# Kernel optimization log

Hardware: AMD Instinct MI355X
Metric: run time of the kernel (lower is better)

The kernel has to match this reference:

```python
import jax, jax.numpy as jnp
import numpy as np

OUT_FEATURES = 4096
IN_FEATURES = 4096
K = 4096
BLOCK_SIZE = 8
NUM_BLOCKS = OUT_FEATURES * IN_FEATURES // BLOCK_SIZE  # 2,097,152
ORIGINAL_NUMEL = OUT_FEATURES * IN_FEATURES


def setup_inputs() -> dict:
    key = jax.random.key(0)
    k1, k2, k3, k4 = jax.random.split(key, 4)
    x = jax.random.normal(k1, (4, 2048, IN_FEATURES), dtype=jnp.float32)
    codebook = jax.random.normal(k2, (K, BLOCK_SIZE), dtype=jnp.float32)
    indices = jax.random.randint(k3, (NUM_BLOCKS,), 0, K, dtype=jnp.int64)
    bias = jax.random.normal(k4, (OUT_FEATURES,), dtype=jnp.float32)
    return {"x": x, "codebook": codebook, "indices": indices, "bias": bias}


def reference(x, codebook, indices, bias):
    # Reconstruct weight from codebook: gather blocks, flatten, slice, reshape.
    reconstructed = codebook[indices]                      # [num_blocks, block_size]
    W = reconstructed.reshape(-1)[:ORIGINAL_NUMEL]
    W = W.reshape(OUT_FEATURES, IN_FEATURES)               # [out, in]
    # F.linear: x @ W^T + bias
    return jnp.einsum('bsi,oi->bso', x, W) + bias
```

## Files before the change

### kernel.cpp

```cpp
#include <hip/hip_runtime.h>
#include <stdint.h>


#define M_DIM 8192
#define N_DIM 4096
#define K_DIM 4096
#define BM 256
#define BN 256
#define BK 64
#define NT (K_DIM / BK)
#define NUM_W_BLOCKS 2097152
#define W_WGS (NUM_W_BLOCKS / 256)
#define X_WGS ((M_DIM * K_DIM / 4) / 256)

typedef __attribute__((ext_vector_type(8))) __bf16 bf16x8;
typedef __attribute__((ext_vector_type(4))) float floatx4;
typedef __attribute__((ext_vector_type(2))) unsigned int uintx2;

__device__ __forceinline__ unsigned int f2bf(float f) {
    unsigned int u = __builtin_bit_cast(unsigned int, f);
    u += 0x7fffu + ((u >> 16) & 1u);
    return u >> 16;
}

__global__ __launch_bounds__(256) void prep_kernel(
    const float* __restrict__ cb, const int* __restrict__ idx,
    uint4* __restrict__ W, const floatx4* __restrict__ x,
    uintx2* __restrict__ xb) {
    const int wg = blockIdx.x;
    if (wg < W_WGS) {
        const int b = wg * 256 + threadIdx.x;
        const int id = __builtin_nontemporal_load(idx + b);
        const float4* s = (const float4*)(cb + ((size_t)id << 3));
        const float4 a = s[0];
        const float4 c = s[1];
        uint4 o;
        o.x = f2bf(a.x) | (f2bf(a.y) << 16);
        o.y = f2bf(a.z) | (f2bf(a.w) << 16);
        o.z = f2bf(c.x) | (f2bf(c.y) << 16);
        o.w = f2bf(c.z) | (f2bf(c.w) << 16);
        W[b] = o;
    } else {
        const size_t t = (size_t)(wg - W_WGS) * 256 + threadIdx.x;
        const floatx4 a = __builtin_nontemporal_load(x + t);
        uintx2 o;
        o.x = f2bf(a.x) | (f2bf(a.y) << 16);
        o.y = f2bf(a.z) | (f2bf(a.w) << 16);
        xb[t] = o;
    }
}

__device__ __forceinline__ void async_copy16(const __bf16* g, __bf16* s) {
    __builtin_amdgcn_global_load_lds(
        (const __attribute__((address_space(1))) unsigned int*)(uintptr_t)g,
        (__attribute__((address_space(3))) unsigned int*)(uintptr_t)s,
        16, 0, 0);
}

#define STAGE(gsrc, arr, slotElems)                                        \
    do {                                                                   \
        async_copy16((gsrc), (arr) + (slotElems) + wave512);               \
        async_copy16((gsrc) + (size_t)128 * K_DIM,                         \
                     (arr) + (slotElems) + 4096 + wave512);                \
    } while (0)

__global__ __launch_bounds__(512, 2) void gemm_bt_kernel(
    const __bf16* __restrict__ A,
    const __bf16* __restrict__ B,
    const float* __restrict__ bias,
    float* __restrict__ C) {
    __shared__ __align__(16) __bf16 sA[4 * 8192];
    __shared__ __align__(16) __bf16 sB[4 * 8192];

    const int tid = threadIdx.x;
    const int wave = tid >> 6;
    const int lane = tid & 63;
    const int wr = wave >> 2;
    const int wc = wave & 3;

    const int flat = blockIdx.x;
    const int swz = (flat & 7) * 64 + (flat >> 3);
    const int m0 = (swz & 31) * BM;
    const int n0 = (swz >> 5) * BN;

    const int srow = tid >> 2;
    const int schunk = ((tid & 3) ^ ((srow >> 1) & 3)) << 3;
    const __bf16* gA = A + (size_t)(m0 + srow) * K_DIM + schunk;
    const __bf16* gB = B + (size_t)(n0 + srow) * K_DIM + schunk;
    const int wave512 = wave << 9;

    const int fr = lane & 15;
    const int roff = fr * 32 + (((lane >> 4) ^ ((fr >> 1) & 3)) << 3);
    const int aBase = wr * 4096 + roff;
    const int bBase = wc * 2048 + roff;

    floatx4 acc[8][4] = {};

    STAGE(gA, sA, 0);
    STAGE(gB, sB, 0);
    STAGE(gA + 32, sA, 8192);
    STAGE(gB + 32, sB, 8192);
    STAGE(gA + 64, sA, 16384);
    STAGE(gB + 64, sB, 16384);
    asm volatile("s_waitcnt vmcnt(4)" ::: "memory");
    __builtin_amdgcn_s_barrier();

    for (int t = 0; t < NT; ++t) {
        const int cs = (t & 1) ? 16384 : 0;
        const int ns = cs ^ 16384;
        const __bf16* sA0 = sA + cs;
        const __bf16* sA1 = sA + cs + 8192;
        const __bf16* sB0 = sB + cs;
        const __bf16* sB1 = sB + cs + 8192;

        bf16x8 af[4], bfr[4];

#pragma unroll
        for (int i = 0; i < 4; ++i)
            af[i] = *(const bf16x8*)(sA0 + aBase + i * 512);
#pragma unroll
        for (int j = 0; j < 4; ++j)
            bfr[j] = *(const bf16x8*)(sB0 + bBase + j * 512);
        if (t + 1 < NT) { STAGE(gA + (size_t)(t + 1) * 64 + 32, sA, ns + 8192); }
        __builtin_amdgcn_s_barrier();
        asm volatile("s_waitcnt lgkmcnt(0)" ::: "memory");
        __builtin_amdgcn_s_setprio(1);
#pragma unroll
        for (int i = 0; i < 4; ++i)
#pragma unroll
            for (int j = 0; j < 4; ++j)
                acc[i][j] = __builtin_amdgcn_mfma_f32_16x16x32_bf16(
                    af[i], bfr[j], acc[i][j], 0, 0, 0);
        __builtin_amdgcn_s_setprio(0);
        __builtin_amdgcn_s_barrier();

#pragma unroll
        for (int i = 0; i < 4; ++i)
            af[i] = *(const bf16x8*)(sA0 + aBase + 2048 + i * 512);
        if (t + 1 < NT) { STAGE(gB + (size_t)(t + 1) * 64 + 32, sB, ns + 8192); }
        __builtin_amdgcn_s_barrier();
        asm volatile("s_waitcnt lgkmcnt(0)" ::: "memory");
        __builtin_amdgcn_s_setprio(1);
#pragma unroll
        for (int i = 0; i < 4; ++i)
#pragma unroll
            for (int j = 0; j < 4; ++j)
                acc[i + 4][j] = __builtin_amdgcn_mfma_f32_16x16x32_bf16(
                    af[i], bfr[j], acc[i + 4][j], 0, 0, 0);
        __builtin_amdgcn_s_setprio(0);
        __builtin_amdgcn_s_barrier();

#pragma unroll
        for (int i = 0; i < 4; ++i)
            af[i] = *(const bf16x8*)(sA1 + aBase + i * 512);
#pragma unroll
        for (int j = 0; j < 4; ++j)
            bfr[j] = *(const bf16x8*)(sB1 + bBase + j * 512);
        if (t + 2 < NT) { STAGE(gA + (size_t)(t + 2) * 64, sA, cs); }
        __builtin_amdgcn_s_barrier();
        asm volatile("s_waitcnt lgkmcnt(0)" ::: "memory");
        __builtin_amdgcn_s_setprio(1);
#pragma unroll
        for (int i = 0; i < 4; ++i)
#pragma unroll
            for (int j = 0; j < 4; ++j)
                acc[i][j] = __builtin_amdgcn_mfma_f32_16x16x32_bf16(
                    af[i], bfr[j], acc[i][j], 0, 0, 0);
        __builtin_amdgcn_s_setprio(0);
        __builtin_amdgcn_s_barrier();

#pragma unroll
        for (int i = 0; i < 4; ++i)
            af[i] = *(const bf16x8*)(sA1 + aBase + 2048 + i * 512);
        if (t + 2 < NT) { STAGE(gB + (size_t)(t + 2) * 64, sB, cs); }
        __builtin_amdgcn_s_barrier();
        asm volatile("s_waitcnt lgkmcnt(0)" ::: "memory");
        __builtin_amdgcn_s_setprio(1);
#pragma unroll
        for (int i = 0; i < 4; ++i)
#pragma unroll
            for (int j = 0; j < 4; ++j)
                acc[i + 4][j] = __builtin_amdgcn_mfma_f32_16x16x32_bf16(
                    af[i], bfr[j], acc[i + 4][j], 0, 0, 0);
        __builtin_amdgcn_s_setprio(0);
        if (t < NT - 2)
            asm volatile("s_waitcnt vmcnt(4)" ::: "memory");
        else
            asm volatile("s_waitcnt vmcnt(0)" ::: "memory");
        __builtin_amdgcn_s_barrier();
    }

    const int crow = (lane >> 4) * 4;
    const int ccol = lane & 15;
#pragma unroll
    for (int j = 0; j < 4; ++j) {
        const int n = n0 + wc * 64 + j * 16 + ccol;
        const float bv = bias[n];
#pragma unroll
        for (int i = 0; i < 8; ++i) {
            const int m = m0 + wr * 128 + i * 16 + crow;
            float* cp = C + (size_t)m * N_DIM + n;
#pragma unroll
            for (int r = 0; r < 4; ++r)
                __builtin_nontemporal_store(acc[i][j][r] + bv,
                                            cp + (size_t)r * N_DIM);
        }
    }
}

extern "C" void kernel_launch(void* const* d_in, const int* in_sizes, int n_in,
                              void* d_out, int out_size, void* d_ws, size_t ws_size,
                              hipStream_t stream) {
    const float* x    = (const float*)d_in[0];
    const float* cb   = (const float*)d_in[1];
    const int*   idx  = (const int*)d_in[2];
    const float* bias = (const float*)d_in[3];
    float* out = (float*)d_out;

    __bf16* Wb = (__bf16*)d_ws;
    __bf16* Xb = (__bf16*)((char*)d_ws + (size_t)N_DIM * K_DIM * sizeof(__bf16));

    prep_kernel<<<W_WGS + X_WGS, 256, 0, stream>>>(
        cb, idx, (uint4*)Wb, (const floatx4*)x, (uintx2*)Xb);

    dim3 grid(M_DIM / BM * (N_DIM / BN));
    gemm_bt_kernel<<<grid, 512, 0, stream>>>(Xb, Wb, bias, out);
}
```

Baseline: 468.9 us.

## Use persistent-style prep loops, remap GEMM tile order, relax vmcnt waits

The prep kernel moves from one element per thread to a fixed grid of workgroups that loop over several elements, and the x conversion now writes 16-byte bf16 chunks instead of 8-byte ones. The GEMM block-to-tile mapping is changed so each XCD works on a compact 4x8 patch of M/N tiles, to improve L2 reuse. The vmcnt waits are relaxed so more async global-to-LDS copies stay in flight between half-iterations. The risk is that the looser waits could break the pipeline ordering or reduce overlap if they are counted wrong.

```diff
diff --git a/kernel.cpp b/kernel.cpp
--- a/kernel.cpp
+++ b/kernel.cpp
@@ -10,12 +10,15 @@
 #define BK 64
 #define NT (K_DIM / BK)
 #define NUM_W_BLOCKS 2097152
-#define W_WGS (NUM_W_BLOCKS / 256)
-#define X_WGS ((M_DIM * K_DIM / 4) / 256)
+
+#define PW_WGS 512
+#define PW_ITERS (NUM_W_BLOCKS / (PW_WGS * 256 * 4))
+#define PX_WGS 2048
+#define PX_OUT (M_DIM * K_DIM / 8)
+#define PX_ITERS (PX_OUT / (PX_WGS * 256))
 
 typedef __attribute__((ext_vector_type(8))) __bf16 bf16x8;
 typedef __attribute__((ext_vector_type(4))) float floatx4;
-typedef __attribute__((ext_vector_type(2))) unsigned int uintx2;
 
 __device__ __forceinline__ unsigned int f2bf(float f) {
     unsigned int u = __builtin_bit_cast(unsigned int, f);
@@ -25,28 +28,42 @@
 
 __global__ __launch_bounds__(256) void prep_kernel(
     const float* __restrict__ cb, const int* __restrict__ idx,
-    uint4* __restrict__ W, const floatx4* __restrict__ x,
-    uintx2* __restrict__ xb) {
+    uint4* __restrict__ W, const float4* __restrict__ x4,
+    uint4* __restrict__ xb4) {
     const int wg = blockIdx.x;
-    if (wg < W_WGS) {
-        const int b = wg * 256 + threadIdx.x;
-        const int id = __builtin_nontemporal_load(idx + b);
-        const float4* s = (const float4*)(cb + ((size_t)id << 3));
-        const float4 a = s[0];
-        const float4 c = s[1];
-        uint4 o;
-        o.x = f2bf(a.x) | (f2bf(a.y) << 16);
-        o.y = f2bf(a.z) | (f2bf(a.w) << 16);
-        o.z = f2bf(c.x) | (f2bf(c.y) << 16);
-        o.w = f2bf(c.z) | (f2bf(c.w) << 16);
-        W[b] = o;
+    const int tid = threadIdx.x;
+    if (wg < PW_WGS) {
+#pragma unroll
+        for (int it = 0; it < PW_ITERS; ++it) {
+#pragma unroll
+            for (int k = 0; k < 4; ++k) {
+                const int b = ((it * PW_WGS + wg) * 4 + k) * 256 + tid;
+                const int id = idx[b];
+                const float4* s = (const float4*)(cb + ((size_t)id << 3));
+                const float4 a = s[0];
+                const float4 c = s[1];
+                uint4 o;
+                o.x = f2bf(a.x) | (f2bf(a.y) << 16);
+                o.y = f2bf(a.z) | (f2bf(a.w) << 16);
+                o.z = f2bf(c.x) | (f2bf(c.y) << 16);
+                o.w = f2bf(c.z) | (f2bf(c.w) << 16);
+                W[b] = o;
+            }
+        }
     } else {
-        const size_t t = (size_t)(wg - W_WGS) * 256 + threadIdx.x;
-        const floatx4 a = __builtin_nontemporal_load(x + t);
-        uintx2 o;
-        o.x = f2bf(a.x) | (f2bf(a.y) << 16);
-        o.y = f2bf(a.z) | (f2bf(a.w) << 16);
-        xb[t] = o;
+        const int xwg = wg - PW_WGS;
+#pragma unroll
+        for (int it = 0; it < PX_ITERS; ++it) {
+            const size_t o = ((size_t)(it * PX_WGS + xwg)) * 256 + tid;
+            const float4 a = x4[2 * o];
+            const float4 c = x4[2 * o + 1];
+            uint4 v;
+            v.x = f2bf(a.x) | (f2bf(a.y) << 16);
+            v.y = f2bf(a.z) | (f2bf(a.w) << 16);
+            v.z = f2bf(c.x) | (f2bf(c.y) << 16);
+            v.w = f2bf(c.z) | (f2bf(c.w) << 16);
+            xb4[o] = v;
+        }
     }
 }
 
@@ -79,9 +96,12 @@
     const int wc = wave & 3;
 
     const int flat = blockIdx.x;
-    const int swz = (flat & 7) * 64 + (flat >> 3);
-    const int m0 = (swz & 31) * BM;
-    const int n0 = (swz >> 5) * BN;
+    const int xcd = flat & 7;
+    const int q = flat >> 3;
+    const int half = q >> 5;
+    const int sq = q & 31;
+    const int m0 = ((xcd & 3) * 8 + half * 4 + (sq & 3)) * BM;
+    const int n0 = ((xcd >> 2) * 8 + (sq >> 2)) * BN;
 
     const int srow = tid >> 2;
     const int schunk = ((tid & 3) ^ ((srow >> 1) & 3)) << 3;
@@ -102,7 +122,7 @@
     STAGE(gB + 32, sB, 8192);
     STAGE(gA + 64, sA, 16384);
     STAGE(gB + 64, sB, 16384);
-    asm volatile("s_waitcnt vmcnt(4)" ::: "memory");
+    asm volatile("s_waitcnt vmcnt(8)" ::: "memory");
     __builtin_amdgcn_s_barrier();
 
     for (int t = 0; t < NT; ++t) {
@@ -148,6 +168,10 @@
                 acc[i + 4][j] = __builtin_amdgcn_mfma_f32_16x16x32_bf16(
                     af[i], bfr[j], acc[i + 4][j], 0, 0, 0);
         __builtin_amdgcn_s_setprio(0);
+        if (t + 1 < NT)
+            asm volatile("s_waitcnt vmcnt(8)" ::: "memory");
+        else
+            asm volatile("s_waitcnt vmcnt(0)" ::: "memory");
         __builtin_amdgcn_s_barrier();
 
 #pragma unroll
@@ -183,7 +207,9 @@
                 acc[i + 4][j] = __builtin_amdgcn_mfma_f32_16x16x32_bf16(
                     af[i], bfr[j], acc[i + 4][j], 0, 0, 0);
         __builtin_amdgcn_s_setprio(0);
-        if (t < NT - 2)
+        if (t + 2 < NT)
+            asm volatile("s_waitcnt vmcnt(8)" ::: "memory");
+        else if (t + 1 < NT)
             asm volatile("s_waitcnt vmcnt(4)" ::: "memory");
         else
             asm volatile("s_waitcnt vmcnt(0)" ::: "memory");
@@ -220,8 +246,8 @@
     __bf16* Wb = (__bf16*)d_ws;
     __bf16* Xb = (__bf16*)((char*)d_ws + (size_t)N_DIM * K_DIM * sizeof(__bf16));
 
-    prep_kernel<<<W_WGS + X_WGS, 256, 0, stream>>>(
-        cb, idx, (uint4*)Wb, (const floatx4*)x, (uintx2*)Xb);
+    prep_kernel<<<PW_WGS + PX_WGS, 256, 0, stream>>>(
+        cb, idx, (uint4*)Wb, (const float4*)x, (uint4*)Xb);
 
     dim3 grid(M_DIM / BM * (N_DIM / BN));
     gemm_bt_kernel<<<grid, 512, 0, stream>>>(Xb, Wb, bias, out);
```

New measurement: 473.1 us. Within noise of the previous version (+0.9%).
